# Kernel optimization log

Measured on AMD Instinct MI355X. Metric: run time of the kernel, lower is better.

## Reference

```python
import jax, jax.numpy as jnp
import numpy as np

KD_T = 4.0
PATCH_NUM = 64
MASK_NUM = 8
BATCH = 256
DIM = 2048
P = PATCH_NUM - MASK_NUM  # 56


def setup_inputs() -> dict:
    key = jax.random.key(0)
    k1, k2, k3 = jax.random.split(key, 3)
    ebg = jax.random.normal(k1, (BATCH, DIM), dtype=jnp.float32)
    ebp = jax.random.normal(k2, (P * BATCH, DIM), dtype=jnp.float32)
    labels = jax.random.randint(k3, (BATCH,), 0, 10, dtype=jnp.int64)
    return {"ebg": ebg, "ebp": ebp, "labels": labels}


def _kl(y_s, y_t, T):
    # Faithful to KLDiv with dim=0 on vectors: softmax over the feature axis,
    # F.kl_div(..., reduction='batchmean') on a length-D vector divides by D.
    D = y_s.shape[-1]
    log_p_s = jax.nn.log_softmax(y_s / T, axis=-1)
    log_p_t = jax.nn.log_softmax(y_t / T, axis=-1)
    p_t = jnp.exp(log_p_t)
    return jnp.sum(p_t * (log_p_t - log_p_s), axis=-1) * (T * T / D)


def reference(ebg, ebp, labels):
    sg = jax.lax.stop_gradient
    ebp_r = ebp.reshape(P, BATCH, DIM)          # [P, B, D]
    ebp_bar = ebp_r.mean(axis=0)                # [B, D]

    # soft_dil_loss: sum over batch of symmetric KD with detached targets
    soft_dil = jnp.sum(_kl(ebg, sg(ebp_bar), KD_T)) + jnp.sum(_kl(ebp_bar, sg(ebg), KD_T))

    # soft_dcl_loss: per (batch, patch) pair on squared differences
    ebp_t = jnp.transpose(ebp_r, (1, 0, 2))     # [B, P, D]
    dg = (ebg[:, None, :] - ebp_t) ** 2         # [B, P, D]
    db = (ebp_bar[:, None, :] - ebp_t) ** 2     # [B, P, D]
    soft_dcl = (jnp.sum(_kl(dg, db, KD_T)) + jnp.sum(_kl(db, dg, KD_T))) / P

    return (soft_dil, soft_dcl)
```

## Files before the change

kernel.cpp:

```cpp
#include <hip/hip_runtime.h>
#include <math.h>

#define DIM    2048
#define BATCH  256
#define PN     56
#define HALF   1024
#define CHUNK  256
#define NCHUNK 4
#define NBLK   512
constexpr float KD_T = 4.0f;

__device__ __forceinline__ float wave_sum(float v) {
#pragma unroll
    for (int o = 32; o > 0; o >>= 1) v += __shfl_xor(v, o, 64);
    return v;
}
__device__ __forceinline__ double wave_sum_d(double v) {
#pragma unroll
    for (int o = 32; o > 0; o >>= 1) v += __shfl_xor(v, o, 64);
    return v;
}

__global__ void __launch_bounds__(256) fused_kernel(const float* __restrict__ ebg,
                                                    const float* __restrict__ ebp,
                                                    float* __restrict__ pdcl,
                                                    float* __restrict__ pdil)
{
    __shared__ float ebp_s[PN * CHUNK];
    __shared__ float bar_s[CHUNK];
    __shared__ float redl[4][4];

    const int t    = threadIdx.x;
    const int lane = t & 63;
    const int wv   = t >> 6;
    const int bid  = blockIdx.x;
    const int b    = bid >> 1;
    const int half = bid & 1;
    const float invT = 1.0f / KD_T;

    float acc[14][4];
#pragma unroll
    for (int i = 0; i < 14; ++i)
#pragma unroll
        for (int j = 0; j < 4; ++j) acc[i][j] = 0.f;

    float dss = 0.f, dts = 0.f, dt1 = 0.f, dt2 = 0.f;

    const size_t browoff = (size_t)b * DIM + (size_t)half * HALF;

    for (int c = 0; c < NCHUNK; ++c) {
        const int base = c * CHUNK;

        const float* ep = ebp + browoff + base + t;
        float bsum = 0.f;
#pragma unroll 14
        for (int p = 0; p < PN; ++p) {
            float v = ep[(size_t)p * (BATCH * DIM)];
            bsum += v;
            ebp_s[p * CHUNK + t] = v;
        }
        float barv = bsum * (1.0f / PN);
        bar_s[t] = barv;
        {
            float g = ebg[browoff + base + t];
            float s = g * invT, tv = barv * invT;
            float es = __expf(s), et = __expf(tv);
            float dd = tv - s;
            dss += es; dts += et;
            dt1 = fmaf(es, dd, dt1);
            dt2 = fmaf(et, dd, dt2);
        }
        __syncthreads();

        const float4 g4 = *(const float4*)(ebg + browoff + base + lane * 4);
        const float4 m4 = *(const float4*)(bar_s + lane * 4);
        const float gs[4] = {g4.x, g4.y, g4.z, g4.w};
        const float ms[4] = {m4.x, m4.y, m4.z, m4.w};
#pragma unroll
        for (int i = 0; i < 14; ++i) {
            const int p = wv * 14 + i;
            float4 e = *(const float4*)(ebp_s + p * CHUNK + lane * 4);
            float es_[4] = {e.x, e.y, e.z, e.w};
#pragma unroll
            for (int k = 0; k < 4; ++k) {
                float dg = gs[k] - es_[k];
                float db = ms[k] - es_[k];
                float a  = dg * dg * invT;
                float cc = db * db * invT;
                float ea = __expf(a), ec = __expf(cc);
                float d  = cc - a;
                acc[i][0] += ea;
                acc[i][1] += ec;
                acc[i][2] = fmaf(ea, d, acc[i][2]);
                acc[i][3] = fmaf(ec, d, acc[i][3]);
            }
        }
        __syncthreads();
    }

#pragma unroll
    for (int i = 0; i < 14; ++i) {
        float a0 = wave_sum(acc[i][0]);
        float a1 = wave_sum(acc[i][1]);
        float a2 = wave_sum(acc[i][2]);
        float a3 = wave_sum(acc[i][3]);
        if (lane == 0) {
            float* q = pdcl + ((size_t)bid * PN + wv * 14 + i) * 4;
            q[0] = a0; q[1] = a1; q[2] = a2; q[3] = a3;
        }
    }
    dss = wave_sum(dss); dts = wave_sum(dts);
    dt1 = wave_sum(dt1); dt2 = wave_sum(dt2);
    if (lane == 0) { redl[wv][0] = dss; redl[wv][1] = dts; redl[wv][2] = dt1; redl[wv][3] = dt2; }
    __syncthreads();
    if (t == 0) {
        float* q = pdil + (size_t)bid * 4;
#pragma unroll
        for (int j = 0; j < 4; ++j)
            q[j] = redl[0][j] + redl[1][j] + redl[2][j] + redl[3][j];
    }
}

__global__ void __launch_bounds__(256) finalize_kernel(const float* __restrict__ pdcl,
                                                       const float* __restrict__ pdil,
                                                       float* __restrict__ out)
{
    __shared__ double sdc[4], sdl[4];
    const int t = threadIdx.x, lane = t & 63, wv = t >> 6;
    const int b = t;

    double dsum = 0.0;
    for (int p = 0; p < PN; ++p) {
        const float* q0 = pdcl + ((size_t)(b * 2 + 0) * PN + p) * 4;
        const float* q1 = pdcl + ((size_t)(b * 2 + 1) * PN + p) * 4;
        double asum = (double)q0[0] + q1[0];
        double csum = (double)q0[1] + q1[1];
        double t1   = (double)q0[2] + q1[2];
        double t2   = (double)q0[3] + q1[3];
        dsum += t2 / csum - t1 / asum;
    }
    const float* r0 = pdil + (size_t)(b * 2 + 0) * 4;
    const float* r1 = pdil + (size_t)(b * 2 + 1) * 4;
    double ss = (double)r0[0] + r1[0];
    double ts = (double)r0[1] + r1[1];
    double u1 = (double)r0[2] + r1[2];
    double u2 = (double)r0[3] + r1[3];
    double lsum = u2 / ts - u1 / ss;

    dsum = wave_sum_d(dsum); lsum = wave_sum_d(lsum);
    if (lane == 0) { sdc[wv] = dsum; sdl[wv] = lsum; }
    __syncthreads();
    if (t == 0) {
        double kT2 = (double)KD_T * KD_T;
        out[0] = (float)((sdl[0] + sdl[1] + sdl[2] + sdl[3]) * (kT2 / DIM));
        out[1] = (float)((sdc[0] + sdc[1] + sdc[2] + sdc[3]) * (kT2 / DIM / PN));
    }
}

extern "C" void kernel_launch(void* const* d_in, const int* in_sizes, int n_in,
                              void* d_out, int out_size, void* d_ws, size_t ws_size,
                              hipStream_t stream) {
    const float* ebg = (const float*)d_in[0];
    const float* ebp = (const float*)d_in[1];

    float* pdcl = (float*)d_ws;
    float* pdil = pdcl + (size_t)NBLK * PN * 4;

    fused_kernel<<<NBLK, 256, 0, stream>>>(ebg, ebp, pdcl, pdil);
    finalize_kernel<<<1, 256, 0, stream>>>(pdcl, pdil, (float*)d_out);
}
```

Baseline: 204.4 us.

## Split rows into quarters with float4 loads and parallelize finalize across patches

Doubles the grid to four blocks per batch row with 128-column chunks, and loads ebp with float4 vector loads over 8 patch rows per pass instead of scalar per-column loads. The patch mean is reduced via a shuffle and a shared-memory reduction across waves, and each half-wave handles one patch row, cutting accumulator registers. The single-block finalize becomes a 56-block pass plus a small final kernel, which removes the serial 56-iteration double loop in exchange for one extra launch.

```diff
diff --git a/kernel.cpp b/kernel.cpp
--- a/kernel.cpp
+++ b/kernel.cpp
@@ -4,15 +4,21 @@
 #define DIM    2048
 #define BATCH  256
 #define PN     56
-#define HALF   1024
-#define CHUNK  256
+#define CHUNK  128
 #define NCHUNK 4
-#define NBLK   512
+#define NQ     4
+#define QCOLS  (CHUNK * NCHUNK)
+#define NBLK   (BATCH * NQ)
 constexpr float KD_T = 4.0f;
 
 __device__ __forceinline__ float wave_sum(float v) {
 #pragma unroll
     for (int o = 32; o > 0; o >>= 1) v += __shfl_xor(v, o, 64);
+    return v;
+}
+__device__ __forceinline__ float half_sum(float v) {
+#pragma unroll
+    for (int o = 16; o > 0; o >>= 1) v += __shfl_xor(v, o, 64);
     return v;
 }
 __device__ __forceinline__ double wave_sum_d(double v) {
@@ -26,60 +32,88 @@
                                                     float* __restrict__ pdcl,
                                                     float* __restrict__ pdil)
 {
-    __shared__ float ebp_s[PN * CHUNK];
-    __shared__ float bar_s[CHUNK];
-    __shared__ float redl[4][4];
+    __shared__ float  ebp_s[PN * CHUNK];
+    __shared__ float4 redbar[4][32];
+    __shared__ float  bar_s[CHUNK];
+    __shared__ float  redl[4][4];
 
     const int t    = threadIdx.x;
     const int lane = t & 63;
     const int wv   = t >> 6;
+    const int sub  = lane >> 5;
+    const int c32  = lane & 31;
     const int bid  = blockIdx.x;
-    const int b    = bid >> 1;
-    const int half = bid & 1;
+    const int b    = bid >> 2;
+    const int q    = bid & (NQ - 1);
     const float invT = 1.0f / KD_T;
 
-    float acc[14][4];
-#pragma unroll
-    for (int i = 0; i < 14; ++i)
-#pragma unroll
-        for (int j = 0; j < 4; ++j) acc[i][j] = 0.f;
+    const size_t rowoff = (size_t)b * DIM + (size_t)q * QCOLS;
+
+    float acc[7][4];
+#pragma unroll
+    for (int j = 0; j < 7; ++j)
+#pragma unroll
+        for (int k = 0; k < 4; ++k) acc[j][k] = 0.f;
 
     float dss = 0.f, dts = 0.f, dt1 = 0.f, dt2 = 0.f;
 
-    const size_t browoff = (size_t)b * DIM + (size_t)half * HALF;
-
     for (int c = 0; c < NCHUNK; ++c) {
-        const int base = c * CHUNK;
-
-        const float* ep = ebp + browoff + base + t;
-        float bsum = 0.f;
-#pragma unroll 14
-        for (int p = 0; p < PN; ++p) {
-            float v = ep[(size_t)p * (BATCH * DIM)];
-            bsum += v;
-            ebp_s[p * CHUNK + t] = v;
-        }
-        float barv = bsum * (1.0f / PN);
-        bar_s[t] = barv;
-        {
-            float g = ebg[browoff + base + t];
-            float s = g * invT, tv = barv * invT;
+        const size_t cb = rowoff + (size_t)c * CHUNK;
+
+        const int prow0 = t >> 5;
+        const int cc4   = (t & 31) * 4;
+        float4 vals[7];
+#pragma unroll
+        for (int it = 0; it < 7; ++it) {
+            const int p = it * 8 + prow0;
+            vals[it] = *(const float4*)(ebp + (size_t)p * (BATCH * DIM) + cb + cc4);
+        }
+        float4 bp = {0.f, 0.f, 0.f, 0.f};
+#pragma unroll
+        for (int it = 0; it < 7; ++it) {
+            const int p = it * 8 + prow0;
+            *(float4*)(ebp_s + p * CHUNK + cc4) = vals[it];
+            bp.x += vals[it].x; bp.y += vals[it].y;
+            bp.z += vals[it].z; bp.w += vals[it].w;
+        }
+        bp.x += __shfl_xor(bp.x, 32, 64);
+        bp.y += __shfl_xor(bp.y, 32, 64);
+        bp.z += __shfl_xor(bp.z, 32, 64);
+        bp.w += __shfl_xor(bp.w, 32, 64);
+        if (c32 == lane) ;
+        if (lane < 32) redbar[wv][lane] = bp;
+        __syncthreads();
+        if (t < 32) {
+            float4 s0 = redbar[0][t], s1 = redbar[1][t],
+                   s2 = redbar[2][t], s3 = redbar[3][t];
+            float4 s;
+            s.x = (s0.x + s1.x + s2.x + s3.x) * (1.0f / PN);
+            s.y = (s0.y + s1.y + s2.y + s3.y) * (1.0f / PN);
+            s.z = (s0.z + s1.z + s2.z + s3.z) * (1.0f / PN);
+            s.w = (s0.w + s1.w + s2.w + s3.w) * (1.0f / PN);
+            *(float4*)(bar_s + t * 4) = s;
+        }
+        __syncthreads();
+
+        if (t < CHUNK) {
+            float g = ebg[cb + t];
+            float m = bar_s[t];
+            float s = g * invT, tv = m * invT;
             float es = __expf(s), et = __expf(tv);
             float dd = tv - s;
             dss += es; dts += et;
             dt1 = fmaf(es, dd, dt1);
             dt2 = fmaf(et, dd, dt2);
         }
-        __syncthreads();
-
-        const float4 g4 = *(const float4*)(ebg + browoff + base + lane * 4);
-        const float4 m4 = *(const float4*)(bar_s + lane * 4);
+
+        const float4 g4 = *(const float4*)(ebg + cb + c32 * 4);
+        const float4 m4 = *(const float4*)(bar_s + c32 * 4);
         const float gs[4] = {g4.x, g4.y, g4.z, g4.w};
         const float ms[4] = {m4.x, m4.y, m4.z, m4.w};
 #pragma unroll
-        for (int i = 0; i < 14; ++i) {
-            const int p = wv * 14 + i;
-            float4 e = *(const float4*)(ebp_s + p * CHUNK + lane * 4);
+        for (int j = 0; j < 7; ++j) {
+            const int row = wv * 14 + 2 * j + sub;
+            float4 e = *(const float4*)(ebp_s + row * CHUNK + c32 * 4);
             float es_[4] = {e.x, e.y, e.z, e.w};
 #pragma unroll
             for (int k = 0; k < 4; ++k) {
@@ -89,24 +123,25 @@
                 float cc = db * db * invT;
                 float ea = __expf(a), ec = __expf(cc);
                 float d  = cc - a;
-                acc[i][0] += ea;
-                acc[i][1] += ec;
-                acc[i][2] = fmaf(ea, d, acc[i][2]);
-                acc[i][3] = fmaf(ec, d, acc[i][3]);
+                acc[j][0] += ea;
+                acc[j][1] += ec;
+                acc[j][2] = fmaf(ea, d, acc[j][2]);
+                acc[j][3] = fmaf(ec, d, acc[j][3]);
             }
         }
         __syncthreads();
     }
 
 #pragma unroll
-    for (int i = 0; i < 14; ++i) {
-        float a0 = wave_sum(acc[i][0]);
-        float a1 = wave_sum(acc[i][1]);
-        float a2 = wave_sum(acc[i][2]);
-        float a3 = wave_sum(acc[i][3]);
-        if (lane == 0) {
-            float* q = pdcl + ((size_t)bid * PN + wv * 14 + i) * 4;
-            q[0] = a0; q[1] = a1; q[2] = a2; q[3] = a3;
+    for (int j = 0; j < 7; ++j) {
+        float a0 = half_sum(acc[j][0]);
+        float a1 = half_sum(acc[j][1]);
+        float a2 = half_sum(acc[j][2]);
+        float a3 = half_sum(acc[j][3]);
+        if (c32 == 0) {
+            const int row = wv * 14 + 2 * j + sub;
+            float* qp = pdcl + (((size_t)row * BATCH + b) * NQ + q) * 4;
+            qp[0] = a0; qp[1] = a1; qp[2] = a2; qp[3] = a3;
         }
     }
     dss = wave_sum(dss); dts = wave_sum(dts);
@@ -114,44 +149,55 @@
     if (lane == 0) { redl[wv][0] = dss; redl[wv][1] = dts; redl[wv][2] = dt1; redl[wv][3] = dt2; }
     __syncthreads();
     if (t == 0) {
-        float* q = pdil + (size_t)bid * 4;
-#pragma unroll
-        for (int j = 0; j < 4; ++j)
-            q[j] = redl[0][j] + redl[1][j] + redl[2][j] + redl[3][j];
-    }
-}
-
-__global__ void __launch_bounds__(256) finalize_kernel(const float* __restrict__ pdcl,
-                                                       const float* __restrict__ pdil,
-                                                       float* __restrict__ out)
+        float* qp = pdil + (size_t)bid * 4;
+#pragma unroll
+        for (int k = 0; k < 4; ++k)
+            qp[k] = redl[0][k] + redl[1][k] + redl[2][k] + redl[3][k];
+    }
+}
+
+__global__ void __launch_bounds__(256) finalize1_kernel(const float* __restrict__ pdcl,
+                                                        double* __restrict__ partial)
+{
+    __shared__ double sd[4];
+    const int p = blockIdx.x, t = threadIdx.x, lane = t & 63, wv = t >> 6;
+    const float* base = pdcl + ((size_t)p * BATCH + t) * NQ * 4;
+    double A = 0.0, C = 0.0, T1 = 0.0, T2 = 0.0;
+#pragma unroll
+    for (int qq = 0; qq < NQ; ++qq) {
+        float4 v = *(const float4*)(base + qq * 4);
+        A += v.x; C += v.y; T1 += v.z; T2 += v.w;
+    }
+    double r = T2 / C - T1 / A;
+    r = wave_sum_d(r);
+    if (lane == 0) sd[wv] = r;
+    __syncthreads();
+    if (t == 0) partial[p] = sd[0] + sd[1] + sd[2] + sd[3];
+}
+
+__global__ void __launch_bounds__(256) finalize2_kernel(const double* __restrict__ partial,
+                                                        const float* __restrict__ pdil,
+                                                        float* __restrict__ out)
 {
     __shared__ double sdc[4], sdl[4];
     const int t = threadIdx.x, lane = t & 63, wv = t >> 6;
-    const int b = t;
-
-    double dsum = 0.0;
-    for (int p = 0; p < PN; ++p) {
-        const float* q0 = pdcl + ((size_t)(b * 2 + 0) * PN + p) * 4;
-        const float* q1 = pdcl + ((size_t)(b * 2 + 1) * PN + p) * 4;
-        double asum = (double)q0[0] + q1[0];
-        double csum = (double)q0[1] + q1[1];
-        double t1   = (double)q0[2] + q1[2];
-        double t2   = (double)q0[3] + q1[3];
-        dsum += t2 / csum - t1 / asum;
-    }
-    const float* r0 = pdil + (size_t)(b * 2 + 0) * 4;
-    const float* r1 = pdil + (size_t)(b * 2 + 1) * 4;
-    double ss = (double)r0[0] + r1[0];
-    double ts = (double)r0[1] + r1[1];
-    double u1 = (double)r0[2] + r1[2];
-    double u2 = (double)r0[3] + r1[3];
-    double lsum = u2 / ts - u1 / ss;
-
-    dsum = wave_sum_d(dsum); lsum = wave_sum_d(lsum);
-    if (lane == 0) { sdc[wv] = dsum; sdl[wv] = lsum; }
+
+    double vd = (t < PN) ? partial[t] : 0.0;
+
+    const float* base = pdil + (size_t)t * NQ * 4;
+    double ss = 0.0, ts = 0.0, u1 = 0.0, u2 = 0.0;
+#pragma unroll
+    for (int qq = 0; qq < NQ; ++qq) {
+        float4 v = *(const float4*)(base + qq * 4);
+        ss += v.x; ts += v.y; u1 += v.z; u2 += v.w;
+    }
+    double vl = u2 / ts - u1 / ss;
+
+    vd = wave_sum_d(vd); vl = wave_sum_d(vl);
+    if (lane == 0) { sdc[wv] = vd; sdl[wv] = vl; }
     __syncthreads();
     if (t == 0) {
-        double kT2 = (double)KD_T * KD_T;
+        const double kT2 = (double)KD_T * KD_T;
         out[0] = (float)((sdl[0] + sdl[1] + sdl[2] + sdl[3]) * (kT2 / DIM));
         out[1] = (float)((sdc[0] + sdc[1] + sdc[2] + sdc[3]) * (kT2 / DIM / PN));
     }
@@ -163,9 +209,11 @@
     const float* ebg = (const float*)d_in[0];
     const float* ebp = (const float*)d_in[1];
 
-    float* pdcl = (float*)d_ws;
-    float* pdil = pdcl + (size_t)NBLK * PN * 4;
+    float*  pdcl    = (float*)d_ws;
+    float*  pdil    = pdcl + (size_t)PN * BATCH * NQ * 4;
+    double* partial = (double*)(pdil + (size_t)NBLK * 4);
 
     fused_kernel<<<NBLK, 256, 0, stream>>>(ebg, ebp, pdcl, pdil);
-    finalize_kernel<<<1, 256, 0, stream>>>(pdcl, pdil, (float*)d_out);
-}
+    finalize1_kernel<<<PN, 256, 0, stream>>>(pdcl, partial);
+    finalize2_kernel<<<1, 256, 0, stream>>>(partial, pdil, (float*)d_out);
+}
```

New measurement: 183.7 us. 1.11x faster.
